# Kernel optimization log

Measured on AMD Instinct MI355X. Metric: run time of the kernel, lower is better.

Reference implementation:

```python
import jax, jax.numpy as jnp
import numpy as np

EPS = 1e-6
BASE_LR = 0.01
MAX_GRAD_NORM = 1.0
CHUNK = 32


def _rms(x, w):
    return x * jax.lax.rsqrt(jnp.mean(x * x, axis=-1, keepdims=True) + EPS) * w


def _mem_fwd(p, x):
    # Memory MLP: linear -> silu -> linear -> RMSNorm -> residual. x: [D]
    h = jax.nn.silu(p['W1'] @ x)
    o = p['W2'] @ h
    return x + _rms(o, p['ln'])


def _loss(p, k, v, w):
    pred = _mem_fwd(p, k)
    return jnp.mean((v - pred) ** 2 * w)


def _binop(a, b):
    # Mamba-like: (a_j*a_i, kv_j + a_j*kv_i)  == torch.addcmul(kv_j, a_j, kv_i)
    (ai, ki), (aj, kj) = a, b
    return (aj * ai, kj + aj * ki)


def _scan_update(past_s, past_m, g, eta, alpha):
    # past_s/past_m: [B,*shape]; g: [B,C,*shape]; eta/alpha: [B,C]
    ext = (1,) * (g.ndim - 2)
    eta_b = eta.reshape(eta.shape + ext)
    alpha_b = alpha.reshape(alpha.shape + ext)
    ones = jnp.ones_like(eta_b[:, :1])
    a = jnp.concatenate([ones, eta_b], axis=1)
    kv = jnp.concatenate([past_s[:, None], -g], axis=1)
    _, s = jax.lax.associative_scan(_binop, (a, kv), axis=1)  # S_t = eta_t*S_{t-1} - g_t
    beta = jnp.concatenate([ones, 1.0 - alpha_b], axis=1)
    mem = jnp.concatenate([past_m[:, None], s[:, 1:]], axis=1)
    _, m = jax.lax.associative_scan(_binop, (beta, mem), axis=1)  # M_t = beta_t*M_{t-1} + S_t
    return s[:, -1], m[:, -1]


def _forward(x, wq, wk, wv, q_norm_w, k_norm_w, alpha_w, theta_w, eta_w, mem_w1, mem_w2, mem_ln):
    B, S, D = x.shape
    NC = S // CHUNK
    params = {'W1': jnp.broadcast_to(mem_w1, (B,) + mem_w1.shape),
              'W2': jnp.broadcast_to(mem_w2, (B,) + mem_w2.shape),
              'ln': jnp.broadcast_to(mem_ln, (B,) + mem_ln.shape)}
    surpr = jax.tree.map(jnp.zeros_like, params)
    xc_all = x.reshape(B, NC, CHUNK, D).transpose(1, 0, 2, 3)  # [NC,B,C,D]
    # per-sample, per-token grad of the TTT loss w.r.t. memory params
    grad_fn = jax.vmap(jax.vmap(jax.grad(_loss), in_axes=(None, 0, 0, 0)),
                       in_axes=(0, 0, 0, 0))

    def step(carry, xc):
        params, surpr = carry
        k = _rms(jax.nn.silu(xc @ wk.T), k_norm_w)      # [B,C,D]
        v = jax.nn.silu(xc @ wv.T)                       # [B,C,D]
        theta = BASE_LR * jax.nn.sigmoid(xc @ theta_w.T)  # [B,C,1] adaptive lr as loss weight
        alpha = jax.nn.sigmoid(xc @ alpha_w.T)[..., 0]     # [B,C] forget gate
        eta = jax.nn.sigmoid(xc @ eta_w.T)[..., 0]         # [B,C] momentum decay
        g = grad_fn(params, k, v, theta)                  # leaves [B,C,*shape]
        # global grad-norm clip per (b, t)
        sq = sum(jnp.sum(gi * gi, axis=tuple(range(2, gi.ndim)))
                 for gi in jax.tree.leaves(g))
        coef = jnp.minimum(MAX_GRAD_NORM / (jnp.sqrt(sq) + 1e-6), 1.0)
        g = jax.tree.map(lambda gi: gi * coef.reshape(coef.shape + (1,) * (gi.ndim - 2)), g)
        new_s, new_p = {}, {}
        for n in params:
            s_n, m_n = _scan_update(surpr[n], params[n], g[n], eta, alpha)
            new_s[n], new_p[n] = s_n, m_n
        return (new_p, new_s), None

    (params, surpr), _ = jax.lax.scan(step, (params, surpr), xc_all)
    # retrieve from the final memory weights
    q = _rms(jax.nn.silu(x @ wq.T), q_norm_w)
    h = jax.nn.silu(jnp.einsum('bsd,bid->bsi', q, params['W1']))
    o = jnp.einsum('bsi,bdi->bsd', h, params['W2'])
    out = q + _rms(o, params['ln'][:, None, :])
    return out


def setup_inputs() -> dict:
    key = jax.random.key(0)
    ks = jax.random.split(key, 12)
    B, S, D, I = 4, 512, 512, 1024

    def xavier(k, shape):
        fan = shape[-1] + shape[-2] if len(shape) > 1 else 2 * shape[-1]
        return jax.random.uniform(k, shape, jnp.float32, -1.0, 1.0) * jnp.sqrt(6.0 / fan)

    return {
        'x': jax.random.normal(ks[0], (B, S, D), jnp.float32),
        'wq': xavier(ks[1], (D, D)),
        'wk': xavier(ks[2], (D, D)),
        'wv': xavier(ks[3], (D, D)),
        'q_norm_w': jnp.ones((D,), jnp.float32),
        'k_norm_w': jnp.ones((D,), jnp.float32),
        'alpha_w': xavier(ks[4], (1, D)),
        'theta_w': xavier(ks[5], (1, D)),
        'eta_w': xavier(ks[6], (1, D)),
        'mem_w1': xavier(ks[7], (I, D)),
        'mem_w2': xavier(ks[8], (D, I)),
        'mem_ln': jnp.ones((D,), jnp.float32),
    }


def reference(x, wq, wk, wv, q_norm_w, k_norm_w, alpha_w, theta_w, eta_w, mem_w1, mem_w2, mem_ln):
    return _forward(x, wq, wk, wv, q_norm_w, k_norm_w, alpha_w, theta_w, eta_w,
                    mem_w1, mem_w2, mem_ln)
```

## Files before the change

kernel.cpp:

```cpp
#include <hip/hip_runtime.h>
#include <hip/hip_bf16.h>

#define B_ 4
#define S_ 512
#define D_ 512
#define I_ 1024
#define C_ 32
#define NC_ 16

#define KBUF (B_*S_*D_)
#define STSZ (B_*I_*D_)
#define HSZ  (B_*I_*C_)
#define DOSZ (B_*C_*D_)
#define OFF_K    0
#define OFF_V    (OFF_K + KBUF)
#define OFF_Q    (OFF_V + KBUF)
#define OFF_TH   (OFF_Q + KBUF)
#define OFF_AL   (OFF_TH + B_*S_)
#define OFF_ET   (OFF_AL + B_*S_)
#define OFF_KN2  (OFF_ET + B_*S_)
#define OFF_SLN  (OFF_KN2 + B_*S_)
#define OFF_MLN  (OFF_SLN + B_*D_)
#define OFF_H2   (OFF_MLN + B_*D_)
#define OFF_Z1   (OFF_H2 + 2*HSZ)
#define OFF_DHP  (OFF_Z1 + HSZ)
#define OFF_DO   (OFF_DHP + HSZ)
#define OFF_DLN  (OFF_DO + DOSZ)
#define OFF_OB   (OFF_DLN + DOSZ)
#define OFF_SLAB (OFF_OB + DOSZ)
#define SLABSTR  256
#define OFF_TICK (OFF_SLAB + NC_*B_*SLABSTR)
#define OFF_FLAG (OFF_TICK + 64)
#define OFF_ORET (OFF_FLAG + 16)
#define OFF_BST  (OFF_ORET + KBUF)
#define OFF_KBFf (OFF_BST + 2*STSZ)
#define OFF_KBTf (OFF_KBFf + KBUF/2)
#define OFF_HIT  (OFF_KBTf + KBUF/2)
#define OFF_HTI  (OFF_HIT + HSZ)
#define OFF_DOB  (OFF_HTI + HSZ)
#define OFF_DOT  (OFF_DOB + DOSZ/2)

typedef __attribute__((ext_vector_type(8))) short s8v;
typedef __attribute__((ext_vector_type(4))) float f4v;

__device__ __forceinline__ float bf2f(__hip_bfloat16 v){ return __bfloat162float(v); }
__device__ __forceinline__ float bfu2f(unsigned short u){ return __uint_as_float(((unsigned)u)<<16); }
__device__ __forceinline__ unsigned short f2bfu(float f){
  unsigned x = __float_as_uint(f);
  return (unsigned short)((x + 0x7FFFu + ((x>>16)&1u)) >> 16);
}
__device__ __forceinline__ float4 u42f4(ushort4 u){
  float4 r; r.x=bfu2f(u.x); r.y=bfu2f(u.y); r.z=bfu2f(u.z); r.w=bfu2f(u.w); return r;
}
__device__ __forceinline__ ushort4 f42u4(float4 v){
  ushort4 r; r.x=f2bfu(v.x); r.y=f2bfu(v.y); r.z=f2bfu(v.z); r.w=f2bfu(v.w); return r;
}
__device__ __forceinline__ float ldin(const void* p, size_t i, int f){
  return f ? ((const float*)p)[i] : bf2f(((const __hip_bfloat16*)p)[i]);
}
__device__ __forceinline__ float4 ld4g(const void* p, size_t i, int f){
  if(f) return ((const float4*)p)[i>>2];
  return u42f4(((const ushort4*)p)[i>>2]);
}
__device__ __forceinline__ void unp8(uint4 u, float* f){
  f[0]=bfu2f((unsigned short)(u.x&0xffffu)); f[1]=bfu2f((unsigned short)(u.x>>16));
// ... 21 lines not shown
}

__global__ void d0_detect(const void* __restrict__ x, float* __restrict__ ws){
  __shared__ int cnt;
  if(threadIdx.x==0) cnt=0;
  __syncthreads();
  unsigned w = ((const unsigned*)x)[(size_t)threadIdx.x*931 + 17];
  int e = (w>>7)&0xFF;
  if(e>=110 && e<=140) atomicAdd(&cnt,1);
  __syncthreads();
  if(threadIdx.x==0) ((int*)(ws+OFF_FLAG))[0] = (cnt<32) ? 1 : 0;
}

__global__ void p0_init(float* __restrict__ ws, const void* __restrict__ w1,
                        const void* __restrict__ w2, const void* __restrict__ ln){
  int f = ((const int*)(ws+OFF_FLAG))[0];
  unsigned short* bst = (unsigned short*)(ws + OFF_BST);
  size_t id = (size_t)blockIdx.x*blockDim.x + threadIdx.x;
  size_t stride = (size_t)gridDim.x*blockDim.x;
  ushort4 z4 = {0,0,0,0};
  for(size_t t4=id; t4<(size_t)(STSZ/4); t4+=stride){
    size_t e4 = t4 % (size_t)(I_*D_/4);
    *(ushort4*)(bst + (size_t)STSZ + t4*4)   = f42u4(ld4g(w1, e4*4, f));
    *(ushort4*)(bst + (size_t)3*STSZ + t4*4) = f42u4(ld4g(w2, e4*4, f));
    *(ushort4*)(bst + t4*4) = z4;
    *(ushort4*)(bst + (size_t)2*STSZ + t4*4) = z4;
  }
  for(size_t t=id; t<(size_t)(B_*D_); t+=stride){
    ws[OFF_MLN+t] = ldin(ln,t % D_,f);
    ws[OFF_SLN+t] = 0.f;
  }
  for(size_t t=id; t<(size_t)(NC_*B_*SLABSTR); t+=stride) ws[OFF_SLAB+t]=0.f;
  int* tick = (int*)(ws + OFF_TICK);
  for(size_t t=id; t<64; t+=stride) tick[t]=0;
}

__global__ void __launch_bounds__(256) cvt_in(const void* __restrict__ x,
                    const void* __restrict__ wk, const void* __restrict__ wv,
                    const void* __restrict__ wq, float* __restrict__ ws){
  int f = ((const int*)(ws+OFF_FLAG))[0];
  unsigned short* xbf = (unsigned short*)(ws + OFF_ORET);
  unsigned short* wbf = (unsigned short*)(ws + OFF_KBFf);
  size_t id = (size_t)blockIdx.x*blockDim.x + threadIdx.x;
  size_t stride = (size_t)gridDim.x*blockDim.x;
  for(size_t t4=id; t4<(size_t)(KBUF/4); t4+=stride)
    *(ushort4*)(xbf + t4*4) = f42u4(ld4g(x, t4*4, f));
  for(size_t t4=id; t4<(size_t)(3*D_*D_/4); t4+=stride){
    int pid = (int)(t4 / (D_*D_/4));
    size_t e4 = t4 % (size_t)(D_*D_/4);
    const void* W = (pid==0)?wk:((pid==1)?wv:wq);
    *(ushort4*)(wbf + t4*4) = f42u4(ld4g(W, e4*4, f));
  }
}

__global__ void __launch_bounds__(256) p1a(float* __restrict__ ws){
  const unsigned short* xbf = (const unsigned short*)(ws + OFF_ORET);
  const unsigned short* wbf = (const unsigned short*)(ws + OFF_KBFf);
  int pid = blockIdx.z;
  float* outp = ws + ((pid==0)?OFF_K:((pid==1)?OFF_V:OFF_Q));
  const unsigned short* W = wbf + (size_t)pid*D_*D_;
  int r0 = blockIdx.x*64, j0 = blockIdx.y*64;
  int w = threadIdx.x>>6, lane = threadIdx.x&63;
  int col = lane&15, lg = lane>>4;
  f4v acc[4] = {{0,0,0,0},{0,0,0,0},{0,0,0,0},{0,0,0,0}};
  for(int k0=0;k0<512;k0+=32){
    s8v bB = __builtin_bit_cast(s8v, *(const uint4*)(W + (size_t)(j0 + w*16 + col)*512 + k0 + lg*8));
    #pragma unroll
// ... 4 lines not shown
  }
  #pragma unroll
  for(int rg=0;rg<4;rg++)
    #pragma unroll
    for(int j=0;j<4;j++){
      float z = acc[rg][j];
      outp[(size_t)(r0 + rg*16 + lg*4 + j)*512 + j0 + w*16 + col] = z/(1.f+expf(-z));
    }
}

__global__ void __launch_bounds__(256) p1b(const void* __restrict__ x,
                    const void* __restrict__ kn,
                    const void* __restrict__ qn,
                    const void* __restrict__ aw,
                    const void* __restrict__ tw,
                    const void* __restrict__ ew,
                    float* __restrict__ ws){
  int f = ((const int*)(ws+OFF_FLAG))[0];
  int tok = blockIdx.x; int tid = threadIdx.x;
  __shared__ float sm[8];
  float* krow = ws + OFF_K + (size_t)tok*512;
  float* qrow = ws + OFF_Q + (size_t)tok*512;
  float a = krow[tid], b = krow[tid+256];
  float ss = blockReduceSum(a*a+b*b, sm);
  float n = rsqrtf(ss*(1.f/512.f) + 1e-6f);
  float k1v = a*n*ldin(kn,tid,f);
  float k2v = b*n*ldin(kn,tid+256,f);
  krow[tid]=k1v; krow[tid+256]=k2v;
  float kn2 = blockReduceSum(k1v*k1v+k2v*k2v, sm);
  if(tid==0) ws[OFF_KN2+tok]=kn2;
  a = qrow[tid]; b = qrow[tid+256];
  ss = blockReduceSum(a*a+b*b, sm);
  n = rsqrtf(ss*(1.f/512.f)+1e-6f);
  qrow[tid]=a*n*ldin(qn,tid,f);
  qrow[tid+256]=b*n*ldin(qn,tid+256,f);
  float x1=ldin(x,(size_t)tok*512+tid,f), x2=ldin(x,(size_t)tok*512+tid+256,f);
  float td = blockReduceSum(x1*ldin(tw,tid,f) + x2*ldin(tw,tid+256,f), sm);
  float ad = blockReduceSum(x1*ldin(aw,tid,f) + x2*ldin(aw,tid+256,f), sm);
  float ed = blockReduceSum(x1*ldin(ew,tid,f) + x2*ldin(ew,tid+256,f), sm);
  if(tid==0){
    ws[OFF_TH+tok] = 0.01f/(1.f+expf(-td));
    ws[OFF_AL+tok] = 1.f/(1.f+expf(-ad));
    ws[OFF_ET+tok] = 1.f/(1.f+expf(-ed));
  }
}

__global__ void __launch_bounds__(256) tr_k(float* __restrict__ ws){
  unsigned short* kbf = (unsigned short*)(ws + OFF_KBFf);
  unsigned short* kbt = (unsigned short*)(ws + OFF_KBTf);
  int b = blockIdx.z, st = blockIdx.y, dt = blockIdx.x;
  int s0 = st*64, d0 = dt*64;
  __shared__ unsigned short t[64][72];
  int tid = threadIdx.x;
  #pragma unroll
  for(int q=0;q<4;q++){
    int idx = tid + q*256; int r = idx>>4, cq = idx&15;
    float4 v = *(const float4*)(ws + OFF_K + ((size_t)(b*512 + s0 + r))*512 + d0 + cq*4);
    ushort4 u; u.x=f2bfu(v.x); u.y=f2bfu(v.y); u.z=f2bfu(v.z); u.w=f2bfu(v.w);
    *(ushort4*)&t[r][cq*4] = u;
    *(ushort4*)(kbf + ((size_t)(b*512 + s0 + r))*512 + d0 + cq*4) = u;
  }
  __syncthreads();
  #pragma unroll
  for(int q=0;q<4;q++){
    int idx = tid + q*256; int d = idx>>4, sq = idx&15;
    ushort4 u; u.x=t[sq*4+0][d]; u.y=t[sq*4+1][d]; u.z=t[sq*4+2][d]; u.w=t[sq*4+3][d];
    *(ushort4*)(kbt + ((size_t)(b*512 + d0 + d))*512 + s0 + sq*4) = u;
  }
}

__global__ void __launch_bounds__(256) k1_w1(float* __restrict__ ws, int c){
  unsigned short* bsw1 = (unsigned short*)(ws + OFF_BST);
  unsigned short* bmw1 = bsw1 + STSZ;
  const unsigned short* kbf = (const unsigned short*)(ws + OFF_KBFf);
  const unsigned short* kbt = (const unsigned short*)(ws + OFF_KBTf);
  int b = blockIdx.y, bx = blockIdx.x, tid = threadIdx.x;
  __shared__ float sE[32], sC[32], scal[3];
  if(c>0){
    const float* slab = ws + OFF_SLAB + ((long)(c-1)*B_ + b)*SLABSTR;
    if(tid<32){ sE[tid]=slab[128+tid]; sC[tid]=slab[160+tid]; }
    if(tid>=32 && tid<35) scal[tid-32]=slab[192+(tid-32)];
  }
  __syncthreads();
  float PE = c>0? scal[0]:1.f, PB = c>0? scal[1]:1.f, Q = c>0? scal[2]:0.f;
  if(bx==64){
    if(c>0){
      for(int d=tid; d<512; d+=256){
        float gE=0,gC=0;
        for(int u=0;u<32;u++){
          float dl = ws[OFF_DLN + ((size_t)(b*32+u))*512 + d];
          gE += sE[u]*dl; gC += sC[u]*dl;
        }
        size_t ix = OFF_SLN + (size_t)b*512 + d;
        float sv=ws[ix], mv=ws[ix + (OFF_MLN-OFF_SLN)];
        ws[ix] = PE*sv - gE;
        ws[ix + (OFF_MLN-OFF_SLN)] = PB*mv + Q*sv - gC;
      }
    }
    return;
  }
  __shared__ __align__(16) float gbf[4][2][16][36];
  __shared__ __align__(16) unsigned short ztile[4][16][40];
  __shared__ __align__(16) float zred[4][16][32];
  __shared__ float hredL[32];
  int w = tid>>6, lane = tid&63;
  int i0 = bx*16;
  int col = lane&15, lg = lane>>4;
  int rr = lane>>2, c0 = (lane&3)*8;
  s8v aE = {}, aC = {};
  if(c>0){
    const float* dp = ws + OFF_DHP + ((size_t)(b*I_ + i0 + col))*32 + lg*8;
    float4 dv0 = *(const float4*)dp;
    float4 dv1 = *(const float4*)(dp+4);
    float dv[8] = {dv0.x,dv0.y,dv0.z,dv0.w,dv1.x,dv1.y,dv1.z,dv1.w};
    #pragma unroll
    for(int j=0;j<8;j++){
      aE[j] = (short)f2bfu(sE[lg*8+j]*dv[j]);
      aC[j] = (short)f2bfu(sC[lg*8+j]*dv[j]);
    }
  }
  f4v zacc0 = {0.f,0.f,0.f,0.f}, zacc1 = {0.f,0.f,0.f,0.f};
  const int d0w = w*128;
  const size_t srowbase = ((size_t)(b*I_ + i0))*512;
  const size_t kprow = (size_t)(c-1)*32;
  for(int sl=0; sl<4; sl++){
    int dbase = d0w + sl*32;
    size_t gaddr = srowbase + (size_t)rr*512 + dbase + c0;
    if(c>0){
      #pragma unroll
      for(int t2=0;t2<2;t2++){
        int dt = dbase + t2*16;
        const unsigned short* kp = kbt + ((size_t)(b*512 + dt + col))*512 + kprow + lg*8;
        s8v kB = __builtin_bit_cast(s8v, *(const uint4*)kp);
        f4v zero4 = {0.f,0.f,0.f,0.f};
        f4v gE4 = __builtin_amdgcn_mfma_f32_16x16x32_bf16(aE, kB, zero4, 0,0,0);
        f4v gC4 = __builtin_amdgcn_mfma_f32_16x16x32_bf16(aC, kB, zero4, 0,0,0);
        #pragma unroll
        for(int j=0;j<4;j++){
          gbf[w][0][lg*4+j][t2*16+col] = gE4[j];
          gbf[w][1][lg*4+j][t2*16+col] = gC4[j];
        }
      }
      uint4 su = *(uint4*)(bsw1 + gaddr);
      uint4 mu = *(uint4*)(bmw1 + gaddr);
      float s8[8], m8[8];
      unp8(su, s8); unp8(mu, m8);
      float ns[8], nmv[8];
      #pragma unroll
      for(int j=0;j<8;j++){
        float ge = gbf[w][0][rr][c0+j];
        float gc = gbf[w][1][rr][c0+j];
        ns[j]  = PE*s8[j] - ge;
        nmv[j] = PB*m8[j] + Q*s8[j] - gc;
      }
      *(uint4*)(bsw1 + gaddr) = pck8(ns);
      uint4 nmu = pck8(nmv);
      *(uint4*)(bmw1 + gaddr) = nmu;
      *(uint4*)&ztile[w][rr][c0] = nmu;
    } else {
      uint4 mu = *(uint4*)(bmw1 + gaddr);
      *(uint4*)&ztile[w][rr][c0] = mu;
    }
    if(c<16){
      s8v mA = __builtin_bit_cast(s8v, *(const uint4*)&ztile[w][col][lg*8]);
      const unsigned short* kc0 = kbf + ((size_t)(b*512 + c*32 + col))*512 + dbase + lg*8;
      s8v kB0 = __builtin_bit_cast(s8v, *(const uint4*)kc0);
      s8v kB1 = __builtin_bit_cast(s8v, *(const uint4*)(kc0 + (size_t)16*512));
      zacc0 = __builtin_amdgcn_mfma_f32_16x16x32_bf16(mA, kB0, zacc0, 0,0,0);
      zacc1 = __builtin_amdgcn_mfma_f32_16x16x32_bf16(mA, kB1, zacc1, 0,0,0);
    }
  }
  if(c<16){
    #pragma unroll
    for(int j=0;j<4;j++){
      zred[w][lg*4+j][col]    = zacc0[j];
      zred[w][lg*4+j][16+col] = zacc1[j];
    }
    if(tid<32) hredL[tid]=0.f;
    __syncthreads();
    unsigned short* hit = (unsigned short*)(ws + OFF_HIT) + (size_t)(c&1)*HSZ;
    unsigned short* hti = (unsigned short*)(ws + OFF_HTI) + (size_t)(c&1)*HSZ;
    #pragma unroll
    for(int e=0;e<2;e++){
      int idx = tid*2+e; int row = idx>>5, t = idx&31;
      float z = zred[0][row][t]+zred[1][row][t]+zred[2][row][t]+zred[3][row][t];
      size_t zb = ((size_t)(b*I_ + i0 + row))*32 + t;
      ws[OFF_Z1+zb] = z;
      float h = z/(1.f+expf(-z));
      unsigned short hb = f2bfu(h);
      hit[zb] = hb;
      hti[((size_t)(b*C_+t))*I_ + i0 + row] = hb;
      atomicAdd(&hredL[t], h*h);
    }
    __syncthreads();
    if(tid<32) atomicAdd(ws + OFF_SLAB + ((size_t)c*B_ + b)*SLABSTR + tid, hredL[tid]);
  }
}

__global__ void __launch_bounds__(256) k2_w2(float* __restrict__ ws, int c){
  unsigned short* bsw2 = (unsigned short*)(ws + OFF_BST) + (size_t)2*STSZ;
  unsigned short* bmw2 = bsw2 + STSZ;
  const unsigned short* hitp = (const unsigned short*)(ws + OFF_HIT) + (size_t)((c-1)&1)*HSZ;
  const unsigned short* htic = (const unsigned short*)(ws + OFF_HTI) + (size_t)(c&1)*HSZ;
  const unsigned short* dotb = (const unsigned short*)(ws + OFF_DOT);
  int b = blockIdx.y, bx = blockIdx.x, tid = threadIdx.x;
  int d0 = bx*16;
  __shared__ float sE[32], sC[32], scal[3];
  __shared__ __align__(16) float gbf[4][2][16][36];
  __shared__ __align__(16) unsigned short ztile[4][16][40];
  __shared__ __align__(16) float ored[4][16][32];
  if(c>0){
    const float* slab = ws + OFF_SLAB + ((long)(c-1)*B_+b)*SLABSTR;
    if(tid<32){ sE[tid]=slab[128+tid]; sC[tid]=slab[160+tid]; }
    if(tid>=32&&tid<35) scal[tid-32]=slab[192+tid-32];
  }
  __syncthreads();
  float PE = c>0?scal[0]:1.f, PB=c>0?scal[1]:1.f, Q=c>0?scal[2]:0.f;
  int w = tid>>6, lane = tid&63;
  int col = lane&15, lg = lane>>4;
  int rr = lane>>2, c0 = (lane&3)*8;
  s8v aE = {}, aC = {};
  if(c>0){
    const unsigned short* dp = dotb + ((size_t)(b*D_ + d0 + col))*32 + lg*8;
    float dv[8]; unp8(*(const uint4*)dp, dv);
    #pragma unroll
    for(int j=0;j<8;j++){
      aE[j] = (short)f2bfu(sE[lg*8+j]*dv[j]);
      aC[j] = (short)f2bfu(sC[lg*8+j]*dv[j]);
    }
  }
  f4v oacc0 = {0.f,0.f,0.f,0.f}, oacc1 = {0.f,0.f,0.f,0.f};
  const size_t srowbase = ((size_t)(b*D_ + d0))*1024;
  size_t ga0 = srowbase + (size_t)rr*1024 + w*256 + c0;
  uint4 su={0,0,0,0}, mu, svn=su, mvn;
  if(c>0) su = *(uint4*)(bsw2 + ga0);
  mu = *(uint4*)(bmw2 + ga0);
  for(int sl=0; sl<8; sl++){
    int ibase = w*256 + sl*32;
    size_t gaddr = srowbase + (size_t)rr*1024 + ibase + c0;
    if(sl<7){
      if(c>0) svn = *(uint4*)(bsw2 + gaddr + 32);
      mvn = *(uint4*)(bmw2 + gaddr + 32);
    }
    if(c>0){
      #pragma unroll
      for(int t2=0;t2<2;t2++){
        const unsigned short* hp = hitp + ((size_t)(b*I_ + ibase + t2*16 + col))*32 + lg*8;
        s8v hB = __builtin_bit_cast(s8v, *(const uint4*)hp);
        f4v zero4 = {0.f,0.f,0.f,0.f};
        f4v gE4 = __builtin_amdgcn_mfma_f32_16x16x32_bf16(aE, hB, zero4, 0,0,0);
        f4v gC4 = __builtin_amdgcn_mfma_f32_16x16x32_bf16(aC, hB, zero4, 0,0,0);
        #pragma unroll
        for(int j=0;j<4;j++){
          gbf[w][0][lg*4+j][t2*16+col] = gE4[j];
          gbf[w][1][lg*4+j][t2*16+col] = gC4[j];
        }
      }
      float s8[8], m8[8];
      unp8(su, s8); unp8(mu, m8);
      float ns[8], nmv[8];
      #pragma unroll
      for(int j=0;j<8;j++){
        ns[j]  = PE*s8[j] - gbf[w][0][rr][c0+j];
        nmv[j] = PB*m8[j] + Q*s8[j] - gbf[w][1][rr][c0+j];
      }
      *(uint4*)(bsw2 + gaddr) = pck8(ns);
      uint4 nmu = pck8(nmv);
      *(uint4*)(bmw2 + gaddr) = nmu;
      *(uint4*)&ztile[w][rr][c0] = nmu;
    } else {
      *(uint4*)&ztile[w][rr][c0] = mu;
    }
    if(c<16){
      s8v mA = __builtin_bit_cast(s8v, *(const uint4*)&ztile[w][col][lg*8]);
      const unsigned short* hb = htic + ((size_t)(b*C_+col))*I_ + ibase + lg*8;
      s8v hB0 = __builtin_bit_cast(s8v, *(const uint4*)hb);
      s8v hB1 = __builtin_bit_cast(s8v, *(const uint4*)(hb + (size_t)16*I_));
      oacc0 = __builtin_amdgcn_mfma_f32_16x16x32_bf16(mA, hB0, oacc0, 0,0,0);
      oacc1 = __builtin_amdgcn_mfma_f32_16x16x32_bf16(mA, hB1, oacc1, 0,0,0);
    }
    su = svn; mu = mvn;
  }
  if(c<16){
    #pragma unroll
    for(int j=0;j<4;j++){
      ored[w][lg*4+j][col]    = oacc0[j];
      ored[w][lg*4+j][16+col] = oacc1[j];
    }
    __syncthreads();
    #pragma unroll
    for(int e=0;e<2;e++){
      int idx = tid*2+e; int row = idx>>5, t = idx&31;
      float o = ored[0][row][t]+ored[1][row][t]+ored[2][row][t]+ored[3][row][t];
      ws[OFF_OB + ((size_t)(b*C_+t))*512 + d0 + row] = o;
    }
  }
}

__global__ void __launch_bounds__(256) k3_rms(float* __restrict__ ws, int c){
  int t = blockIdx.x, b = blockIdx.y, tid=threadIdx.x;
  __shared__ float sm[8];
  int tok = b*S_ + c*32 + t;
  const float* orow = ws + OFF_OB + ((size_t)(b*32+t))*512;
  const float* krow = ws + OFF_K + (size_t)tok*512;
  const float* vrow = ws + OFF_V + (size_t)tok*512;
  const float* lrow = ws + OFF_MLN + (size_t)b*512;
  float th = ws[OFF_TH + tok];
  float o1=orow[tid], o2=orow[tid+256];
  float mu = blockReduceSum(o1*o1+o2*o2, sm)*(1.f/512.f);
  float n = rsqrtf(mu + 1e-6f);
  float l1=lrow[tid], l2=lrow[tid+256];
  float k1=krow[tid], k2=krow[tid+256];
  float v1=vrow[tid], v2=vrow[tid+256];
  float c2 = 2.f*th*(1.f/512.f);
  float u1 = c2*(k1 + o1*n*l1 - v1);
  float u2 = c2*(k2 + o2*n*l2 - v2);
  float s1 = blockReduceSum(u1*l1*o1 + u2*l2*o2, sm);
  float dln1 = u1*o1*n, dln2v = u2*o2*n;
  float f = n*n*n*s1*(1.f/512.f);
  float do1 = n*l1*u1 - f*o1;
  float do2 = n*l2*u2 - f*o2;
  float don2 = blockReduceSum(do1*do1+do2*do2, sm);
  float dl2s = blockReduceSum(dln1*dln1+dln2v*dln2v, sm);
  float* dorow = ws + OFF_DO + ((size_t)(b*32+t))*512;
  float* dlrow = ws + OFF_DLN + ((size_t)(b*32+t))*512;
  dorow[tid]=do1; dorow[tid+256]=do2;
  dlrow[tid]=dln1; dlrow[tid+256]=dln2v;
  unsigned short* dob = (unsigned short*)(ws + OFF_DOB);
  unsigned short* dotb = (unsigned short*)(ws + OFF_DOT);
  dob[((size_t)(b*C_+t))*512 + tid]       = f2bfu(do1);
  dob[((size_t)(b*C_+t))*512 + tid + 256] = f2bfu(do2);
  dotb[((size_t)(b*D_ + tid))*32 + t]       = f2bfu(do1);
  dotb[((size_t)(b*D_ + tid + 256))*32 + t] = f2bfu(do2);
  if(tid==0){
    float* slab = ws + OFF_SLAB + ((size_t)c*B_+b)*SLABSTR;
    slab[64+t]=don2; slab[96+t]=dl2s;
  }
}

__global__ void __launch_bounds__(256) k4_dh(float* __restrict__ ws, int c){
  unsigned short* bmw2 = (unsigned short*)(ws + OFF_BST) + (size_t)3*STSZ;
  const unsigned short* dob = (const unsigned short*)(ws + OFF_DOB);
  int bx = blockIdx.x, b = blockIdx.y, tid = threadIdx.x;
  int i0 = bx*16;
  __shared__ unsigned short m2u[16][520];
  __shared__ __align__(16) float dred[4][16][32];
  __shared__ float red[32], coefl[32], bsufl[32];
  __shared__ int lastf;
  #pragma unroll
  for(int q=0;q<4;q++){
    int idx = tid + q*256; int d = idx>>1, half = idx&1;
    uint4 v = *(const uint4*)(bmw2 + ((size_t)(b*D_+d))*1024 + i0 + half*8);
    unsigned short tmp[8]; *(uint4*)tmp = v;
    #pragma unroll
    for(int jj=0;jj<8;jj++) m2u[half*8+jj][d] = tmp[jj];
  }
  if(tid<32) red[tid]=0.f;
  __syncthreads();
  int w = tid>>6, lane = tid&63;
  int col = lane&15, lg = lane>>4;
  f4v acc0 = {0.f,0.f,0.f,0.f}, acc1 = {0.f,0.f,0.f,0.f};
  #pragma unroll
  for(int ks=0;ks<4;ks++){
    int k0 = w*128 + ks*32;
    s8v mA = __builtin_bit_cast(s8v, *(const uint4*)&m2u[col][k0 + lg*8]);
    const unsigned short* dp = dob + ((size_t)(b*C_+col))*512 + k0 + lg*8;
    s8v dB0 = __builtin_bit_cast(s8v, *(const uint4*)dp);
    s8v dB1 = __builtin_bit_cast(s8v, *(const uint4*)(dp + (size_t)16*512));
    acc0 = __builtin_amdgcn_mfma_f32_16x16x32_bf16(mA, dB0, acc0, 0,0,0);
    acc1 = __builtin_amdgcn_mfma_f32_16x16x32_bf16(mA, dB1, acc1, 0,0,0);
  }
  #pragma unroll
  for(int j=0;j<4;j++){
    dred[w][lg*4+j][col]    = acc0[j];
    dred[w][lg*4+j][16+col] = acc1[j];
  }
  __syncthreads();
  #pragma unroll
  for(int e=0;e<2;e++){
    int idx = tid*2+e; int row = idx>>5, t = idx&31;
    float dh = dred[0][row][t]+dred[1][row][t]+dred[2][row][t]+dred[3][row][t];
    size_t zb = ((size_t)(b*I_ + i0 + row))*32 + t;
    float z = ws[OFF_Z1+zb];
    float s = 1.f/(1.f+expf(-z));
    float dp_ = dh * s*(1.f + z*(1.f-s));
    ws[OFF_DHP+zb] = dp_;
    atomicAdd(&red[t], dp_*dp_);
  }
  __syncthreads();
  float* slab = ws + OFF_SLAB + ((size_t)c*B_+b)*SLABSTR;
  if(tid<32) atomicAdd(&slab[32+tid], red[tid]);
// ... 6 lines not shown
  __syncthreads();
  if(!lastf) return;
  if(tid<32){
    float sqd = atomicAdd(&slab[32+tid], 0.f);
    float hn  = atomicAdd(&slab[0+tid], 0.f);
    float don2 = slab[64+tid], dl2 = slab[96+tid];
    float kn2 = ws[OFF_KN2 + b*S_ + c*32 + tid];
    float sq = sqd*kn2 + don2*hn + dl2;
    coefl[tid] = fminf(1.f/(sqrtf(sq)+1e-6f), 1.f);
  }
  __syncthreads();
  if(tid==0){
    const float* eta = ws + OFF_ET + b*S_ + c*32;
    const float* alp = ws + OFF_AL + b*S_ + c*32;
    float Esuf=1.f, Bsuf=1.f, cu=1.f;
    for(int u=31;u>=0;u--){
      if(u<31){
        float e1 = eta[u+1], b1 = 1.f-alp[u+1];
        Esuf *= e1; Bsuf *= b1;
        cu = Bsuf + e1*cu;
      }
      bsufl[u]=Bsuf;
      slab[128+u] = Esuf*coefl[u];
      slab[160+u] = cu*coefl[u];
    }
    float PE = Esuf*eta[0];
    float PB = Bsuf*(1.f-alp[0]);
    float Q=0.f, Epre=1.f;
    for(int t2=0;t2<32;t2++){ Epre *= eta[t2]; Q += bsufl[t2]*Epre; }
    slab[192]=PE; slab[193]=PB; slab[194]=Q;
  }
}

__global__ void __launch_bounds__(256) cvt_q(float* __restrict__ ws){
  unsigned short* qbf = (unsigned short*)(ws + OFF_V);
  size_t id = (size_t)blockIdx.x*blockDim.x + threadIdx.x;
  float4 v = *(const float4*)(ws + OFF_Q + id*4);
  *(ushort4*)(qbf + id*4) = f42u4(v);
}

__global__ void __launch_bounds__(256) r1_gemm(float* __restrict__ ws){
  const unsigned short* qbf = (const unsigned short*)(ws + OFF_V);
  const unsigned short* bmw1 = (const unsigned short*)(ws + OFF_BST) + STSZ;
  unsigned short* hqb = (unsigned short*)(ws + OFF_K);
  int b = blockIdx.z;
  int s0 = blockIdx.x*64, i0 = blockIdx.y*64;
  int w = threadIdx.x>>6, lane = threadIdx.x&63;
  int col = lane&15, lg = lane>>4;
  const unsigned short* qb = qbf + (size_t)b*S_*D_;
  const unsigned short* w1b = bmw1 + (size_t)b*I_*D_;
  f4v acc[4] = {{0,0,0,0},{0,0,0,0},{0,0,0,0},{0,0,0,0}};
  for(int k0=0;k0<512;k0+=32){
    s8v bB = __builtin_bit_cast(s8v, *(const uint4*)(w1b + (size_t)(i0 + w*16 + col)*512 + k0 + lg*8));
    #pragma unroll
    for(int rg=0;rg<4;rg++){
      s8v aA = __builtin_bit_cast(s8v, *(const uint4*)(qb + (size_t)(s0 + rg*16 + col)*512 + k0 + lg*8));
      acc[rg] = __builtin_amdgcn_mfma_f32_16x16x32_bf16(aA, bB, acc[rg], 0,0,0);
    }
  }
  unsigned short* hb = hqb + (size_t)b*S_*I_;
  #pragma unroll
  for(int rg=0;rg<4;rg++)
    #pragma unroll
    for(int j=0;j<4;j++){
      float z = acc[rg][j];
      hb[(size_t)(s0 + rg*16 + lg*4 + j)*1024 + i0 + w*16 + col] = f2bfu(z/(1.f+expf(-z)));
    }
}

__global__ void __launch_bounds__(256) r2_gemm(float* __restrict__ ws){
  const unsigned short* hqb = (const unsigned short*)(ws + OFF_K);
  const unsigned short* bmw2 = (const unsigned short*)(ws + OFF_BST) + (size_t)3*STSZ;
  int b=blockIdx.z;
  int s0=blockIdx.x*64, d0=blockIdx.y*64;
  int w = threadIdx.x>>6, lane = threadIdx.x&63;
// ... 33 lines not shown
  if(f){
    ((float*)out)[(size_t)tok*512+tid]     = r1v;
    ((float*)out)[(size_t)tok*512+tid+256] = r2v;
  } else {
    ((__hip_bfloat16*)out)[(size_t)tok*512+tid]     = __float2bfloat16(r1v);
    ((__hip_bfloat16*)out)[(size_t)tok*512+tid+256] = __float2bfloat16(r2v);
  }
}

extern "C" void kernel_launch(void* const* d_in, const int* in_sizes, int n_in,
                              void* d_out, int out_size, void* d_ws, size_t ws_size,
                              hipStream_t stream) {
  const void* x  = d_in[0];
  const void* wq = d_in[1];
  const void* wk = d_in[2];
  const void* wv = d_in[3];
  const void* qn = d_in[4];
  const void* kn = d_in[5];
  const void* aw = d_in[6];
  const void* tw = d_in[7];
  const void* ew = d_in[8];
  const void* w1 = d_in[9];
  const void* w2 = d_in[10];
  const void* ln = d_in[11];
  float* ws = (float*)d_ws;

  d0_detect<<<1,64,0,stream>>>(x, ws);
  p0_init<<<2048,256,0,stream>>>(ws, w1, w2, ln);
  cvt_in<<<2048,256,0,stream>>>(x, wk, wv, wq, ws);
  p1a<<<dim3(32,8,3),256,0,stream>>>(ws);
  p1b<<<2048,256,0,stream>>>(x, kn, qn, aw, tw, ew, ws);
  tr_k<<<dim3(8,8,4),256,0,stream>>>(ws);
  for(int c=0;c<=16;c++){
    k1_w1<<<dim3(65,4),256,0,stream>>>(ws, c);
    k2_w2<<<dim3(32,4),256,0,stream>>>(ws, c);
    if(c<16){
      k3_rms<<<dim3(32,4),256,0,stream>>>(ws, c);
      k4_dh<<<dim3(64,4),256,0,stream>>>(ws, c);
    }
  }
  cvt_q<<<1024,256,0,stream>>>(ws);
  r1_gemm<<<dim3(8,16,4),256,0,stream>>>(ws);
  r2_gemm<<<dim3(8,8,4),256,0,stream>>>(ws);
  r3_out<<<2048,256,0,stream>>>(ws, d_out);
}
```

Baseline: 1.056 ms.

## Fuse per-chunk kernel pairs with intra-grid atomic tickets and drop cvt_q

Merges the W1 and W2 update kernels into one launch, and the RMS-backward and dH kernels into another. Inside each launch, consumer blocks spin on per-batch atomic counters until producer blocks have written the data they depend on. This halves the per-chunk kernel launches and lets independent work (the W2 state update, the M2 tile load) overlap with the producers. The q bf16 conversion also moves into p1b, removing the separate cvt_q pass. The spin-wait relies on all producer blocks being co-resident, which the grid sizes and launch bounds of 2 blocks per SM are meant to ensure, otherwise it could deadlock.

```diff
diff --git a/kernel.cpp b/kernel.cpp
--- a/kernel.cpp
+++ b/kernel.cpp
@@ -30,7 +30,8 @@
 #define OFF_SLAB (OFF_OB + DOSZ)
 #define SLABSTR  256
 #define OFF_TICK (OFF_SLAB + NC_*B_*SLABSTR)
-#define OFF_FLAG (OFF_TICK + 64)
+#define OFF_TK2  (OFF_TICK + 64)
+#define OFF_FLAG (OFF_TK2 + 128)
 #define OFF_ORET (OFF_FLAG + 16)
 #define OFF_BST  (OFF_ORET + KBUF)
 #define OFF_KBFf (OFF_BST + 2*STSZ)
@@ -118,7 +119,7 @@
   }
   for(size_t t=id; t<(size_t)(NC_*B_*SLABSTR); t+=stride) ws[OFF_SLAB+t]=0.f;
   int* tick = (int*)(ws + OFF_TICK);
-  for(size_t t=id; t<64; t+=stride) tick[t]=0;
+  for(size_t t=id; t<192; t+=stride) tick[t]=0;
 }
 
 __global__ void __launch_bounds__(256) cvt_in(const void* __restrict__ x,
@@ -189,8 +190,12 @@
   a = qrow[tid]; b = qrow[tid+256];
   ss = blockReduceSum(a*a+b*b, sm);
   n = rsqrtf(ss*(1.f/512.f)+1e-6f);
-  qrow[tid]=a*n*ldin(qn,tid,f);
-  qrow[tid+256]=b*n*ldin(qn,tid+256,f);
+  float q1 = a*n*ldin(qn,tid,f);
+  float q2 = b*n*ldin(qn,tid+256,f);
+  qrow[tid]=q1; qrow[tid+256]=q2;
+  unsigned short* qbf = (unsigned short*)(ws + OFF_ORET + KBUF/2);
+  qbf[(size_t)tok*512+tid]     = f2bfu(q1);
+  qbf[(size_t)tok*512+tid+256] = f2bfu(q2);
   float x1=ldin(x,(size_t)tok*512+tid,f), x2=ldin(x,(size_t)tok*512+tid+256,f);
   float td = blockReduceSum(x1*ldin(tw,tid,f) + x2*ldin(tw,tid+256,f), sm);
   float ad = blockReduceSum(x1*ldin(aw,tid,f) + x2*ldin(aw,tid+256,f), sm);
@@ -226,13 +231,20 @@
   }
 }
 
-__global__ void __launch_bounds__(256) k1_w1(float* __restrict__ ws, int c){
+__global__ void __launch_bounds__(256,2) fused12(float* __restrict__ ws, int c){
   unsigned short* bsw1 = (unsigned short*)(ws + OFF_BST);
   unsigned short* bmw1 = bsw1 + STSZ;
+  unsigned short* bsw2 = bsw1 + (size_t)2*STSZ;
+  unsigned short* bmw2 = bsw1 + (size_t)3*STSZ;
   const unsigned short* kbf = (const unsigned short*)(ws + OFF_KBFf);
   const unsigned short* kbt = (const unsigned short*)(ws + OFF_KBTf);
   int b = blockIdx.y, bx = blockIdx.x, tid = threadIdx.x;
+  int* tkA = (int*)(ws + OFF_TK2);
   __shared__ float sE[32], sC[32], scal[3];
+  __shared__ __align__(16) float gbf[4][2][16][36];
+  __shared__ __align__(16) unsigned short ztile[4][16][40];
+  __shared__ __align__(16) float xred[4][16][32];
+  __shared__ float hredL[32];
   if(c>0){
     const float* slab = ws + OFF_SLAB + ((long)(c-1)*B_ + b)*SLABSTR;
     if(tid<32){ sE[tid]=slab[128+tid]; sC[tid]=slab[160+tid]; }
@@ -240,6 +252,9 @@
   }
   __syncthreads();
   float PE = c>0? scal[0]:1.f, PB = c>0? scal[1]:1.f, Q = c>0? scal[2]:0.f;
+  int w = tid>>6, lane = tid&63;
+  int col = lane&15, lg = lane>>4;
+  int rr = lane>>2, c0 = (lane&3)*8;
   if(bx==64){
     if(c>0){
       for(int d=tid; d<512; d+=256){
@@ -256,150 +271,128 @@
     }
     return;
   }
-  __shared__ __align__(16) float gbf[4][2][16][36];
-  __shared__ __align__(16) unsigned short ztile[4][16][40];
-  __shared__ __align__(16) float zred[4][16][32];
-  __shared__ float hredL[32];
-  int w = tid>>6, lane = tid&63;
-  int i0 = bx*16;
-  int col = lane&15, lg = lane>>4;
-  int rr = lane>>2, c0 = (lane&3)*8;
-  s8v aE = {}, aC = {};
-  if(c>0){
-    const float* dp = ws + OFF_DHP + ((size_t)(b*I_ + i0 + col))*32 + lg*8;
-    float4 dv0 = *(const float4*)dp;
-    float4 dv1 = *(const float4*)(dp+4);
-    float dv[8] = {dv0.x,dv0.y,dv0.z,dv0.w,dv1.x,dv1.y,dv1.z,dv1.w};
-    #pragma unroll
-    for(int j=0;j<8;j++){
-      aE[j] = (short)f2bfu(sE[lg*8+j]*dv[j]);
-      aC[j] = (short)f2bfu(sC[lg*8+j]*dv[j]);
-    }
-  }
-  f4v zacc0 = {0.f,0.f,0.f,0.f}, zacc1 = {0.f,0.f,0.f,0.f};
-  const int d0w = w*128;
-  const size_t srowbase = ((size_t)(b*I_ + i0))*512;
-  const size_t kprow = (size_t)(c-1)*32;
-  for(int sl=0; sl<4; sl++){
-    int dbase = d0w + sl*32;
-    size_t gaddr = srowbase + (size_t)rr*512 + dbase + c0;
+  if(bx<64){
+    int i0 = bx*16;
+    s8v aE = {}, aC = {};
     if(c>0){
-      #pragma unroll
-      for(int t2=0;t2<2;t2++){
-        int dt = dbase + t2*16;
-        const unsigned short* kp = kbt + ((size_t)(b*512 + dt + col))*512 + kprow + lg*8;
-        s8v kB = __builtin_bit_cast(s8v, *(const uint4*)kp);
-        f4v zero4 = {0.f,0.f,0.f,0.f};
-        f4v gE4 = __builtin_amdgcn_mfma_f32_16x16x32_bf16(aE, kB, zero4, 0,0,0);
-        f4v gC4 = __builtin_amdgcn_mfma_f32_16x16x32_bf16(aC, kB, zero4, 0,0,0);
-        #pragma unroll
-        for(int j=0;j<4;j++){
-          gbf[w][0][lg*4+j][t2*16+col] = gE4[j];
-          gbf[w][1][lg*4+j][t2*16+col] = gC4[j];
-        }
-      }
-      uint4 su = *(uint4*)(bsw1 + gaddr);
-      uint4 mu = *(uint4*)(bmw1 + gaddr);
-      float s8[8], m8[8];
-      unp8(su, s8); unp8(mu, m8);
-      float ns[8], nmv[8];
+      const float* dp = ws + OFF_DHP + ((size_t)(b*I_ + i0 + col))*32 + lg*8;
+      float4 dv0 = *(const float4*)dp;
+      float4 dv1 = *(const float4*)(dp+4);
+      float dv[8] = {dv0.x,dv0.y,dv0.z,dv0.w,dv1.x,dv1.y,dv1.z,dv1.w};
       #pragma unroll
       for(int j=0;j<8;j++){
-        float ge = gbf[w][0][rr][c0+j];
-        float gc = gbf[w][1][rr][c0+j];
-        ns[j]  = PE*s8[j] - ge;
-        nmv[j] = PB*m8[j] + Q*s8[j] - gc;
-      }
-      *(uint4*)(bsw1 + gaddr) = pck8(ns);
-      uint4 nmu = pck8(nmv);
-      *(uint4*)(bmw1 + gaddr) = nmu;
-      *(uint4*)&ztile[w][rr][c0] = nmu;
-    } else {
-      uint4 mu = *(uint4*)(bmw1 + gaddr);
-      *(uint4*)&ztile[w][rr][c0] = mu;
+        aE[j] = (short)f2bfu(sE[lg*8+j]*dv[j]);
+        aC[j] = (short)f2bfu(sC[lg*8+j]*dv[j]);
+      }
+    }
+    f4v zacc0 = {0.f,0.f,0.f,0.f}, zacc1 = {0.f,0.f,0.f,0.f};
+    const int d0w = w*128;
+    const size_t srowbase = ((size_t)(b*I_ + i0))*512;
+    const size_t kprow = (size_t)(c-1)*32;
+    for(int sl=0; sl<4; sl++){
+      int dbase = d0w + sl*32;
+      size_t gaddr = srowbase + (size_t)rr*512 + dbase + c0;
+      if(c>0){
+        #pragma unroll
+        for(int t2=0;t2<2;t2++){
+          int dt = dbase + t2*16;
+          const unsigned short* kp = kbt + ((size_t)(b*512 + dt + col))*512 + kprow + lg*8;
+          s8v kB = __builtin_bit_cast(s8v, *(const uint4*)kp);
+          f4v zero4 = {0.f,0.f,0.f,0.f};
+          f4v gE4 = __builtin_amdgcn_mfma_f32_16x16x32_bf16(aE, kB, zero4, 0,0,0);
+          f4v gC4 = __builtin_amdgcn_mfma_f32_16x16x32_bf16(aC, kB, zero4, 0,0,0);
+          #pragma unroll
+          for(int j=0;j<4;j++){
+            gbf[w][0][lg*4+j][t2*16+col] = gE4[j];
+            gbf[w][1][lg*4+j][t2*16+col] = gC4[j];
+          }
+        }
+        uint4 su = *(uint4*)(bsw1 + gaddr);
+        uint4 mu = *(uint4*)(bmw1 + gaddr);
+        float s8[8], m8[8];
+        unp8(su, s8); unp8(mu, m8);
+        float ns[8], nmv[8];
+        #pragma unroll
+        for(int j=0;j<8;j++){
+          float ge = gbf[w][0][rr][c0+j];
+          float gc = gbf[w][1][rr][c0+j];
+          ns[j]  = PE*s8[j] - ge;
+          nmv[j] = PB*m8[j] + Q*s8[j] - gc;
+        }
+        *(uint4*)(bsw1 + gaddr) = pck8(ns);
+        uint4 nmu = pck8(nmv);
+        *(uint4*)(bmw1 + gaddr) = nmu;
+        *(uint4*)&ztile[w][rr][c0] = nmu;
+      } else {
+        uint4 mu = *(uint4*)(bmw1 + gaddr);
+        *(uint4*)&ztile[w][rr][c0] = mu;
+      }
+      if(c<16){
+        s8v mA = __builtin_bit_cast(s8v, *(const uint4*)&ztile[w][col][lg*8]);
+        const unsigned short* kc0 = kbf + ((size_t)(b*512 + c*32 + col))*512 + dbase + lg*8;
+        s8v kB0 = __builtin_bit_cast(s8v, *(const uint4*)kc0);
+        s8v kB1 = __builtin_bit_cast(s8v, *(const uint4*)(kc0 + (size_t)16*512));
+        zacc0 = __builtin_amdgcn_mfma_f32_16x16x32_bf16(mA, kB0, zacc0, 0,0,0);
+        zacc1 = __builtin_amdgcn_mfma_f32_16x16x32_bf16(mA, kB1, zacc1, 0,0,0);
+      }
     }
     if(c<16){
-      s8v mA = __builtin_bit_cast(s8v, *(const uint4*)&ztile[w][col][lg*8]);
-      const unsigned short* kc0 = kbf + ((size_t)(b*512 + c*32 + col))*512 + dbase + lg*8;
-      s8v kB0 = __builtin_bit_cast(s8v, *(const uint4*)kc0);
-      s8v kB1 = __builtin_bit_cast(s8v, *(const uint4*)(kc0 + (size_t)16*512));
-      zacc0 = __builtin_amdgcn_mfma_f32_16x16x32_bf16(mA, kB0, zacc0, 0,0,0);
-      zacc1 = __builtin_amdgcn_mfma_f32_16x16x32_bf16(mA, kB1, zacc1, 0,0,0);
-    }
-  }
-  if(c<16){
-    #pragma unroll
-    for(int j=0;j<4;j++){
-      zred[w][lg*4+j][col]    = zacc0[j];
-      zred[w][lg*4+j][16+col] = zacc1[j];
-    }
-    if(tid<32) hredL[tid]=0.f;
-    __syncthreads();
-    unsigned short* hit = (unsigned short*)(ws + OFF_HIT) + (size_t)(c&1)*HSZ;
-    unsigned short* hti = (unsigned short*)(ws + OFF_HTI) + (size_t)(c&1)*HSZ;
-    #pragma unroll
-    for(int e=0;e<2;e++){
-      int idx = tid*2+e; int row = idx>>5, t = idx&31;
-      float z = zred[0][row][t]+zred[1][row][t]+zred[2][row][t]+zred[3][row][t];
-      size_t zb = ((size_t)(b*I_ + i0 + row))*32 + t;
-      ws[OFF_Z1+zb] = z;
-      float h = z/(1.f+expf(-z));
-      unsigned short hb = f2bfu(h);
-      hit[zb] = hb;
-      hti[((size_t)(b*C_+t))*I_ + i0 + row] = hb;
-      atomicAdd(&hredL[t], h*h);
-    }
-    __syncthreads();
-    if(tid<32) atomicAdd(ws + OFF_SLAB + ((size_t)c*B_ + b)*SLABSTR + tid, hredL[tid]);
-  }
-}
-
-__global__ void __launch_bounds__(256) k2_w2(float* __restrict__ ws, int c){
-  unsigned short* bsw2 = (unsigned short*)(ws + OFF_BST) + (size_t)2*STSZ;
-  unsigned short* bmw2 = bsw2 + STSZ;
+      #pragma unroll
+      for(int j=0;j<4;j++){
+        xred[w][lg*4+j][col]    = zacc0[j];
+        xred[w][lg*4+j][16+col] = zacc1[j];
+      }
+      if(tid<32) hredL[tid]=0.f;
+      __syncthreads();
+      unsigned short* hit = (unsigned short*)(ws + OFF_HIT) + (size_t)(c&1)*HSZ;
+      unsigned short* hti = (unsigned short*)(ws + OFF_HTI) + (size_t)(c&1)*HSZ;
+      #pragma unroll
+      for(int e=0;e<2;e++){
+        int idx = tid*2+e; int row = idx>>5, t = idx&31;
+        float z = xred[0][row][t]+xred[1][row][t]+xred[2][row][t]+xred[3][row][t];
+        size_t zb = ((size_t)(b*I_ + i0 + row))*32 + t;
+        ws[OFF_Z1+zb] = z;
+        float h = z/(1.f+expf(-z));
+        unsigned short hb = f2bfu(h);
+        hit[zb] = hb;
+        hti[((size_t)(b*C_+t))*I_ + i0 + row] = hb;
+        atomicAdd(&hredL[t], h*h);
+      }
+      __syncthreads();
+      if(tid<32) atomicAdd(ws + OFF_SLAB + ((size_t)c*B_ + b)*SLABSTR + tid, hredL[tid]);
+      __threadfence();
+      __syncthreads();
+      if(tid==0) atomicAdd(&tkA[c*B_+b], 1);
+    }
+    return;
+  }
+  int d0 = (bx-65)*16;
   const unsigned short* hitp = (const unsigned short*)(ws + OFF_HIT) + (size_t)((c-1)&1)*HSZ;
   const unsigned short* htic = (const unsigned short*)(ws + OFF_HTI) + (size_t)(c&1)*HSZ;
   const unsigned short* dotb = (const unsigned short*)(ws + OFF_DOT);
-  int b = blockIdx.y, bx = blockIdx.x, tid = threadIdx.x;
-  int d0 = bx*16;
-  __shared__ float sE[32], sC[32], scal[3];
-  __shared__ __align__(16) float gbf[4][2][16][36];
-  __shared__ __align__(16) unsigned short ztile[4][16][40];
-  __shared__ __align__(16) float ored[4][16][32];
+  const size_t srowbase = ((size_t)(b*D_ + d0))*1024;
   if(c>0){
-    const float* slab = ws + OFF_SLAB + ((long)(c-1)*B_+b)*SLABSTR;
-    if(tid<32){ sE[tid]=slab[128+tid]; sC[tid]=slab[160+tid]; }
-    if(tid>=32&&tid<35) scal[tid-32]=slab[192+tid-32];
-  }
-  __syncthreads();
-  float PE = c>0?scal[0]:1.f, PB=c>0?scal[1]:1.f, Q=c>0?scal[2]:0.f;
-  int w = tid>>6, lane = tid&63;
-  int col = lane&15, lg = lane>>4;
-  int rr = lane>>2, c0 = (lane&3)*8;
-  s8v aE = {}, aC = {};
-  if(c>0){
-    const unsigned short* dp = dotb + ((size_t)(b*D_ + d0 + col))*32 + lg*8;
-    float dv[8]; unp8(*(const uint4*)dp, dv);
-    #pragma unroll
-    for(int j=0;j<8;j++){
-      aE[j] = (short)f2bfu(sE[lg*8+j]*dv[j]);
-      aC[j] = (short)f2bfu(sC[lg*8+j]*dv[j]);
-    }
-  }
-  f4v oacc0 = {0.f,0.f,0.f,0.f}, oacc1 = {0.f,0.f,0.f,0.f};
-  const size_t srowbase = ((size_t)(b*D_ + d0))*1024;
-  size_t ga0 = srowbase + (size_t)rr*1024 + w*256 + c0;
-  uint4 su={0,0,0,0}, mu, svn=su, mvn;
-  if(c>0) su = *(uint4*)(bsw2 + ga0);
-  mu = *(uint4*)(bmw2 + ga0);
-  for(int sl=0; sl<8; sl++){
-    int ibase = w*256 + sl*32;
-    size_t gaddr = srowbase + (size_t)rr*1024 + ibase + c0;
-    if(sl<7){
-      if(c>0) svn = *(uint4*)(bsw2 + gaddr + 32);
-      mvn = *(uint4*)(bmw2 + gaddr + 32);
-    }
-    if(c>0){
+    s8v aE = {}, aC = {};
+    {
+      const unsigned short* dp = dotb + ((size_t)(b*D_ + d0 + col))*32 + lg*8;
+      float dv[8]; unp8(*(const uint4*)dp, dv);
+      #pragma unroll
+      for(int j=0;j<8;j++){
+        aE[j] = (short)f2bfu(sE[lg*8+j]*dv[j]);
+        aC[j] = (short)f2bfu(sC[lg*8+j]*dv[j]);
+      }
+    }
+    size_t ga0 = srowbase + (size_t)rr*1024 + w*256 + c0;
+    uint4 su = *(uint4*)(bsw2 + ga0);
+    uint4 mu = *(uint4*)(bmw2 + ga0);
+    uint4 svn = su, mvn = mu;
+    for(int sl=0; sl<8; sl++){
+      int ibase = w*256 + sl*32;
+      size_t gaddr = srowbase + (size_t)rr*1024 + ibase + c0;
+      if(sl<7){
+        svn = *(uint4*)(bsw2 + gaddr + 32);
+        mvn = *(uint4*)(bmw2 + gaddr + 32);
+      }
       #pragma unroll
       for(int t2=0;t2<2;t2++){
         const unsigned short* hp = hitp + ((size_t)(b*I_ + ibase + t2*16 + col))*32 + lg*8;
@@ -422,88 +415,96 @@
         nmv[j] = PB*m8[j] + Q*s8[j] - gbf[w][1][rr][c0+j];
       }
       *(uint4*)(bsw2 + gaddr) = pck8(ns);
-      uint4 nmu = pck8(nmv);
-      *(uint4*)(bmw2 + gaddr) = nmu;
-      *(uint4*)&ztile[w][rr][c0] = nmu;
-    } else {
-      *(uint4*)&ztile[w][rr][c0] = mu;
-    }
-    if(c<16){
-      s8v mA = __builtin_bit_cast(s8v, *(const uint4*)&ztile[w][col][lg*8]);
-      const unsigned short* hb = htic + ((size_t)(b*C_+col))*I_ + ibase + lg*8;
-      s8v hB0 = __builtin_bit_cast(s8v, *(const uint4*)hb);
-      s8v hB1 = __builtin_bit_cast(s8v, *(const uint4*)(hb + (size_t)16*I_));
+      *(uint4*)(bmw2 + gaddr) = pck8(nmv);
+      su = svn; mu = mvn;
+    }
+  }
+  if(c<16){
+    if(tid==0){
+      while(atomicAdd(&tkA[c*B_+b], 0) < 64) __builtin_amdgcn_s_sleep(8);
+    }
+    __syncthreads();
+    __threadfence();
+    f4v oacc0 = {0.f,0.f,0.f,0.f}, oacc1 = {0.f,0.f,0.f,0.f};
+    const unsigned short* mrowb = bmw2 + ((size_t)(b*D_ + d0 + col))*1024;
+    #pragma unroll
+    for(int sl=0; sl<8; sl++){
+      int ibase = w*256 + sl*32;
+      s8v mA = __builtin_bit_cast(s8v, *(const uint4*)(mrowb + ibase + lg*8));
+      const unsigned short* hb2 = htic + ((size_t)(b*C_+col))*I_ + ibase + lg*8;
+      s8v hB0 = __builtin_bit_cast(s8v, *(const uint4*)hb2);
+      s8v hB1 = __builtin_bit_cast(s8v, *(const uint4*)(hb2 + (size_t)16*I_));
       oacc0 = __builtin_amdgcn_mfma_f32_16x16x32_bf16(mA, hB0, oacc0, 0,0,0);
       oacc1 = __builtin_amdgcn_mfma_f32_16x16x32_bf16(mA, hB1, oacc1, 0,0,0);
     }
-    su = svn; mu = mvn;
-  }
-  if(c<16){
     #pragma unroll
     for(int j=0;j<4;j++){
-      ored[w][lg*4+j][col]    = oacc0[j];
-      ored[w][lg*4+j][16+col] = oacc1[j];
+      xred[w][lg*4+j][col]    = oacc0[j];
+      xred[w][lg*4+j][16+col] = oacc1[j];
     }
     __syncthreads();
     #pragma unroll
     for(int e=0;e<2;e++){
       int idx = tid*2+e; int row = idx>>5, t = idx&31;
-      float o = ored[0][row][t]+ored[1][row][t]+ored[2][row][t]+ored[3][row][t];
+      float o = xred[0][row][t]+xred[1][row][t]+xred[2][row][t]+xred[3][row][t];
       ws[OFF_OB + ((size_t)(b*C_+t))*512 + d0 + row] = o;
     }
   }
 }
 
-__global__ void __launch_bounds__(256) k3_rms(float* __restrict__ ws, int c){
-  int t = blockIdx.x, b = blockIdx.y, tid=threadIdx.x;
-  __shared__ float sm[8];
-  int tok = b*S_ + c*32 + t;
-  const float* orow = ws + OFF_OB + ((size_t)(b*32+t))*512;
-  const float* krow = ws + OFF_K + (size_t)tok*512;
-  const float* vrow = ws + OFF_V + (size_t)tok*512;
-  const float* lrow = ws + OFF_MLN + (size_t)b*512;
-  float th = ws[OFF_TH + tok];
-  float o1=orow[tid], o2=orow[tid+256];
-  float mu = blockReduceSum(o1*o1+o2*o2, sm)*(1.f/512.f);
-  float n = rsqrtf(mu + 1e-6f);
-  float l1=lrow[tid], l2=lrow[tid+256];
-  float k1=krow[tid], k2=krow[tid+256];
-  float v1=vrow[tid], v2=vrow[tid+256];
-  float c2 = 2.f*th*(1.f/512.f);
-  float u1 = c2*(k1 + o1*n*l1 - v1);
-  float u2 = c2*(k2 + o2*n*l2 - v2);
-  float s1 = blockReduceSum(u1*l1*o1 + u2*l2*o2, sm);
-  float dln1 = u1*o1*n, dln2v = u2*o2*n;
-  float f = n*n*n*s1*(1.f/512.f);
-  float do1 = n*l1*u1 - f*o1;
-  float do2 = n*l2*u2 - f*o2;
-  float don2 = blockReduceSum(do1*do1+do2*do2, sm);
-  float dl2s = blockReduceSum(dln1*dln1+dln2v*dln2v, sm);
-  float* dorow = ws + OFF_DO + ((size_t)(b*32+t))*512;
-  float* dlrow = ws + OFF_DLN + ((size_t)(b*32+t))*512;
-  dorow[tid]=do1; dorow[tid+256]=do2;
-  dlrow[tid]=dln1; dlrow[tid+256]=dln2v;
-  unsigned short* dob = (unsigned short*)(ws + OFF_DOB);
-  unsigned short* dotb = (unsigned short*)(ws + OFF_DOT);
-  dob[((size_t)(b*C_+t))*512 + tid]       = f2bfu(do1);
-  dob[((size_t)(b*C_+t))*512 + tid + 256] = f2bfu(do2);
-  dotb[((size_t)(b*D_ + tid))*32 + t]       = f2bfu(do1);
-  dotb[((size_t)(b*D_ + tid + 256))*32 + t] = f2bfu(do2);
-  if(tid==0){
-    float* slab = ws + OFF_SLAB + ((size_t)c*B_+b)*SLABSTR;
-    slab[64+t]=don2; slab[96+t]=dl2s;
-  }
-}
-
-__global__ void __launch_bounds__(256) k4_dh(float* __restrict__ ws, int c){
+__global__ void __launch_bounds__(256,2) fused34(float* __restrict__ ws, int c){
   unsigned short* bmw2 = (unsigned short*)(ws + OFF_BST) + (size_t)3*STSZ;
   const unsigned short* dob = (const unsigned short*)(ws + OFF_DOB);
   int bx = blockIdx.x, b = blockIdx.y, tid = threadIdx.x;
   int i0 = bx*16;
+  int* tkB = (int*)(ws + OFF_TK2) + 64;
   __shared__ unsigned short m2u[16][520];
   __shared__ __align__(16) float dred[4][16][32];
   __shared__ float red[32], coefl[32], bsufl[32];
+  __shared__ float smr[8];
   __shared__ int lastf;
+  if(bx<32){
+    int t = bx;
+    int tok = b*S_ + c*32 + t;
+    const float* orow = ws + OFF_OB + ((size_t)(b*32+t))*512;
+    const float* krow = ws + OFF_K + (size_t)tok*512;
+    const float* vrow = ws + OFF_V + (size_t)tok*512;
+    const float* lrow = ws + OFF_MLN + (size_t)b*512;
+    float th = ws[OFF_TH + tok];
+    float o1=orow[tid], o2=orow[tid+256];
+    float mu = blockReduceSum(o1*o1+o2*o2, smr)*(1.f/512.f);
+    float n = rsqrtf(mu + 1e-6f);
+    float l1=lrow[tid], l2=lrow[tid+256];
+    float k1=krow[tid], k2=krow[tid+256];
+    float v1=vrow[tid], v2=vrow[tid+256];
+    float c2 = 2.f*th*(1.f/512.f);
+    float u1 = c2*(k1 + o1*n*l1 - v1);
+    float u2 = c2*(k2 + o2*n*l2 - v2);
+    float s1 = blockReduceSum(u1*l1*o1 + u2*l2*o2, smr);
+    float dln1 = u1*o1*n, dln2v = u2*o2*n;
+    float fr = n*n*n*s1*(1.f/512.f);
+    float do1 = n*l1*u1 - fr*o1;
+    float do2 = n*l2*u2 - fr*o2;
+    float don2 = blockReduceSum(do1*do1+do2*do2, smr);
+    float dl2s = blockReduceSum(dln1*dln1+dln2v*dln2v, smr);
+    float* dorow = ws + OFF_DO + ((size_t)(b*32+t))*512;
+    float* dlrow = ws + OFF_DLN + ((size_t)(b*32+t))*512;
+    dorow[tid]=do1; dorow[tid+256]=do2;
+    dlrow[tid]=dln1; dlrow[tid+256]=dln2v;
+    unsigned short* dobw = (unsigned short*)(ws + OFF_DOB);
+    unsigned short* dotw = (unsigned short*)(ws + OFF_DOT);
+    dobw[((size_t)(b*C_+t))*512 + tid]       = f2bfu(do1);
+    dobw[((size_t)(b*C_+t))*512 + tid + 256] = f2bfu(do2);
+    dotw[((size_t)(b*D_ + tid))*32 + t]       = f2bfu(do1);
+    dotw[((size_t)(b*D_ + tid + 256))*32 + t] = f2bfu(do2);
+    if(tid==0){
+      float* slab = ws + OFF_SLAB + ((size_t)c*B_+b)*SLABSTR;
+      slab[64+t]=don2; slab[96+t]=dl2s;
+    }
+    __threadfence();
+    __syncthreads();
+    if(tid==0) atomicAdd(&tkB[c*B_+b], 1);
+  }
   #pragma unroll
   for(int q=0;q<4;q++){
     int idx = tid + q*256; int d = idx>>1, half = idx&1;
@@ -514,6 +515,11 @@
   }
   if(tid<32) red[tid]=0.f;
   __syncthreads();
+  if(tid==0){
+    while(atomicAdd(&tkB[c*B_+b], 0) < 32) __builtin_amdgcn_s_sleep(8);
+  }
+  __syncthreads();
+  __threadfence();
   int w = tid>>6, lane = tid&63;
   int col = lane&15, lg = lane>>4;
   f4v acc0 = {0.f,0.f,0.f,0.f}, acc1 = {0.f,0.f,0.f,0.f};
@@ -586,15 +592,8 @@
   }
 }
 
-__global__ void __launch_bounds__(256) cvt_q(float* __restrict__ ws){
-  unsigned short* qbf = (unsigned short*)(ws + OFF_V);
-  size_t id = (size_t)blockIdx.x*blockDim.x + threadIdx.x;
-  float4 v = *(const float4*)(ws + OFF_Q + id*4);
-  *(ushort4*)(qbf + id*4) = f42u4(v);
-}
-
 __global__ void __launch_bounds__(256) r1_gemm(float* __restrict__ ws){
-  const unsigned short* qbf = (const unsigned short*)(ws + OFF_V);
+  const unsigned short* qbf = (const unsigned short*)(ws + OFF_ORET + KBUF/2);
   const unsigned short* bmw1 = (const unsigned short*)(ws + OFF_BST) + STSZ;
   unsigned short* hqb = (unsigned short*)(ws + OFF_K);
   int b = blockIdx.z;
@@ -694,14 +693,9 @@
   p1b<<<2048,256,0,stream>>>(x, kn, qn, aw, tw, ew, ws);
   tr_k<<<dim3(8,8,4),256,0,stream>>>(ws);
   for(int c=0;c<=16;c++){
-    k1_w1<<<dim3(65,4),256,0,stream>>>(ws, c);
-    k2_w2<<<dim3(32,4),256,0,stream>>>(ws, c);
-    if(c<16){
-      k3_rms<<<dim3(32,4),256,0,stream>>>(ws, c);
-      k4_dh<<<dim3(64,4),256,0,stream>>>(ws, c);
-    }
-  }
-  cvt_q<<<1024,256,0,stream>>>(ws);
+    fused12<<<dim3(97,B_),256,0,stream>>>(ws, c);
+    if(c<16) fused34<<<dim3(64,B_),256,0,stream>>>(ws, c);
+  }
   r1_gemm<<<dim3(8,16,4),256,0,stream>>>(ws);
   r2_gemm<<<dim3(8,8,4),256,0,stream>>>(ws);
   r3_out<<<2048,256,0,stream>>>(ws, d_out);
```

New measurement: 2.338 ms. 2.21x slower.
